# Kernel optimization log

Hardware: AMD Instinct MI355X
Metric: run time of the kernel (lower is better)

The kernel has to match this reference:

```python
import jax, jax.numpy as jnp
import numpy as np

B, T, D, H = 2048, 512, 1, 36


def _lstm_dir(x, Wih, Whh, bih, bhh, reverse):
    # x: [B,T,Din]; Wih: [4H,Din]; Whh: [4H,H]. PyTorch gate order: i,f,g,o.
    # Precompute input projection for all timesteps (hoisted out of the scan).
    xp = jnp.einsum('btd,gd->btg', x, Wih) + (bih + bhh)  # [B,T,4H]
    xp = jnp.swapaxes(xp, 0, 1)  # [T,B,4H]
    if reverse:
        xp = xp[::-1]
    h0 = jnp.zeros((x.shape[0], Whh.shape[1]), x.dtype)

    def step(carry, xt):
        h, c = carry
        z = xt + h @ Whh.T  # [B,4H]
        i, f, g, o = jnp.split(z, 4, axis=-1)
        c = jax.nn.sigmoid(f) * c + jax.nn.sigmoid(i) * jnp.tanh(g)
        h = jax.nn.sigmoid(o) * jnp.tanh(c)
        return (h, c), h

    _, hs = jax.lax.scan(step, (h0, h0), xp)  # hs: [T,B,H]
    if reverse:
        hs = hs[::-1]
    return jnp.swapaxes(hs, 0, 1)  # [B,T,H]


def _bilstm_layer(x, pf, pr):
    hf = _lstm_dir(x, *pf, reverse=False)
    hr = _lstm_dir(x, *pr, reverse=True)
    return jnp.concatenate([hf, hr], axis=-1)  # [B,T,2H]


def setup_inputs() -> dict:
    key = jax.random.key(0)
    ks = jax.random.split(key, 20)
    bound = 1.0 / np.sqrt(H)  # PyTorch LSTM/Linear uniform init bound

    def u(k, shape):
        return jax.random.uniform(k, shape, jnp.float32, -bound, bound)

    inp = {"x": jax.random.normal(ks[0], (B, T, D), jnp.float32)}
    # layer 0 (input size D), forward and reverse directions
    inp["Wih0f"] = u(ks[1], (4 * H, D)); inp["Whh0f"] = u(ks[2], (4 * H, H))
    inp["bih0f"] = u(ks[3], (4 * H,));  inp["bhh0f"] = u(ks[4], (4 * H,))
    inp["Wih0r"] = u(ks[5], (4 * H, D)); inp["Whh0r"] = u(ks[6], (4 * H, H))
    inp["bih0r"] = u(ks[7], (4 * H,));  inp["bhh0r"] = u(ks[8], (4 * H,))
    # layer 1 (input size 2H)
    inp["Wih1f"] = u(ks[9], (4 * H, 2 * H)); inp["Whh1f"] = u(ks[10], (4 * H, H))
    inp["bih1f"] = u(ks[11], (4 * H,));      inp["bhh1f"] = u(ks[12], (4 * H,))
    inp["Wih1r"] = u(ks[13], (4 * H, 2 * H)); inp["Whh1r"] = u(ks[14], (4 * H, H))
    inp["bih1r"] = u(ks[15], (4 * H,));       inp["bhh1r"] = u(ks[16], (4 * H,))
    # fc head: Linear(2H -> 1)
    inp["fcW"] = u(ks[17], (1, 2 * H))
    inp["fcb"] = u(ks[18], (1,))
    return inp


def reference(x, Wih0f, Whh0f, bih0f, bhh0f, Wih0r, Whh0r, bih0r, bhh0r,
              Wih1f, Whh1f, bih1f, bhh1f, Wih1r, Whh1r, bih1r, bhh1r,
              fcW, fcb):
    out = _bilstm_layer(x, (Wih0f, Whh0f, bih0f, bhh0f),
                        (Wih0r, Whh0r, bih0r, bhh0r))
    out = _bilstm_layer(out, (Wih1f, Whh1f, bih1f, bhh1f),
                        (Wih1r, Whh1r, bih1r, bhh1r))
    return out[:, -1, :] @ fcW.T + fcb  # [B,1]
```

## Files before the change

### kernel.cpp

```cpp
#include <hip/hip_runtime.h>
#include <cstdint>

#define Hn 36
#define G4 144
#define TT 512
#define BB 2048

__device__ __forceinline__ float sigf(float x) { return 1.0f / (1.0f + __expf(-x)); }
__device__ __forceinline__ float tanh_fast(float x) {
    float e = __expf(2.0f * x);
    return 1.0f - 2.0f / (e + 1.0f);
}

#define REP9(M, P)  M(P,0) M(P,1) M(P,2) M(P,3) M(P,4) M(P,5) M(P,6) M(P,7) M(P,8)
#define DECLQ(P, i) float P##i##x, P##i##y, P##i##z, P##i##w;
#define LOADQ(P, i) { float4 _t = wp[i]; P##i##x = _t.x; P##i##y = _t.y; P##i##z = _t.z; P##i##w = _t.w; }
#define PINQ(P, i)  asm volatile("" : "+v"(P##i##x), "+v"(P##i##y), "+v"(P##i##z), "+v"(P##i##w));
#define FMAQ(P, i)                                                        \
    {  float4 hv = *(const float4*)&hb[(i) * 4];                          \
       z0 = fmaf(P##i##x, hv.x, z0); z1 = fmaf(P##i##y, hv.y, z1);        \
       z2 = fmaf(P##i##z, hv.z, z2); z3 = fmaf(P##i##w, hv.w, z3); }

#define DOT4Q(P, i)                                                       \
    {   float4 hA = *(const float4*)&hbb[0 * 40 + (i) * 4];               \
        A0 = fmaf(P##i##x, hA.x, A0); A1 = fmaf(P##i##y, hA.y, A1);       \
        A2 = fmaf(P##i##z, hA.z, A2); A3 = fmaf(P##i##w, hA.w, A3);       \
        float4 hB = *(const float4*)&hbb[1 * 40 + (i) * 4];               \
        B0 = fmaf(P##i##x, hB.x, B0); B1 = fmaf(P##i##y, hB.y, B1);       \
        B2 = fmaf(P##i##z, hB.z, B2); B3 = fmaf(P##i##w, hB.w, B3);       \
        float4 hC = *(const float4*)&hbb[2 * 40 + (i) * 4];               \
        C0 = fmaf(P##i##x, hC.x, C0); C1 = fmaf(P##i##y, hC.y, C1);       \
        C2 = fmaf(P##i##z, hC.z, C2); C3 = fmaf(P##i##w, hC.w, C3);       \
        float4 hD = *(const float4*)&hbb[3 * 40 + (i) * 4];               \
        D0 = fmaf(P##i##x, hD.x, D0); D1 = fmaf(P##i##y, hD.y, D1);       \
        D2 = fmaf(P##i##z, hD.z, D2); D3 = fmaf(P##i##w, hD.w, D3); }

#define DOT36(W, H, Z0, Z1, Z2, Z3)                        \
    do {                                                   \
        _Pragma("unroll") for (int _k = 0; _k < 9; ++_k) { \
            float4 hv = *(const float4*)&(H)[_k * 4];      \
            Z0 = fmaf((W)[_k * 4 + 0], hv.x, Z0);          \
            Z1 = fmaf((W)[_k * 4 + 1], hv.y, Z1);          \
            Z2 = fmaf((W)[_k * 4 + 2], hv.z, Z2);          \
            Z3 = fmaf((W)[_k * 4 + 3], hv.w, Z3);          \
        }                                                  \
    } while (0)

#define DOT72(W, H, Z0, Z1, Z2, Z3)                         \
    do {                                                    \
        _Pragma("unroll") for (int _k = 0; _k < 18; ++_k) { \
            float4 hv = *(const float4*)&(H)[_k * 4];       \
            Z0 = fmaf((W)[_k * 4 + 0], hv.x, Z0);           \
            Z1 = fmaf((W)[_k * 4 + 1], hv.y, Z1);           \
            Z2 = fmaf((W)[_k * 4 + 2], hv.z, Z2);           \
            Z3 = fmaf((W)[_k * 4 + 3], hv.w, Z3);           \
        }                                                   \
    } while (0)

#define SG1 4
#define NTK1 (SG1 * G4)
__global__ __launch_bounds__(NTK1) void l0rev_kernel(
    const float* __restrict__ x,
    const float* __restrict__ Wih, const float* __restrict__ Whh,
    const float* __restrict__ bih, const float* __restrict__ bhh,
    float* __restrict__ h0r)
{
    const int tid = threadIdx.x;
    const int cc  = tid / G4;
    const int g   = tid % G4;
    const int b   = blockIdx.x * SG1 + cc;

    __shared__ float xs[SG1][TT];
    __shared__ float hs[SG1][40];
    __shared__ float zs[SG1][G4];

    for (int i = g; i < TT; i += G4) xs[cc][i] = x[(size_t)b * TT + i];

    REP9(DECLQ, R)
    {
        const float4* wp = (const float4*)(Whh + g * Hn);
        REP9(LOADQ, R)
    }
    float wx   = Wih[g];
    float bias = bih[g] + bhh[g];
    REP9(PINQ, R)
    asm volatile("" : "+v"(wx), "+v"(bias));

    if (g < 40) hs[cc][g] = 0.0f;
    float c = 0.0f;
    __syncthreads();

    float* dst = h0r + (size_t)b * TT * Hn;

    for (int s = 0; s < TT; ++s) {
        const int t = TT - 1 - s;
        float z0 = fmaf(xs[cc][t], wx, bias), z1 = 0.f, z2 = 0.f, z3 = 0.f;
        {
            const float* hb = hs[cc];
            REP9(FMAQ, R)
        }
        zs[cc][g] = (z0 + z1) + (z2 + z3);
        __syncthreads();
        if (g < Hn) {
            float zi = zs[cc][g], zf = zs[cc][g + 36], zg = zs[cc][g + 72], zo = zs[cc][g + 108];
            c = sigf(zf) * c + sigf(zi) * tanh_fast(zg);
            float h = sigf(zo) * tanh_fast(c);
            hs[cc][g] = h;
            dst[(size_t)t * Hn + g] = h;
        }
        __syncthreads();
    }
}

#define SG2 4
#define NT2 576
__global__ __launch_bounds__(NT2) void fused_fl_kernel(
    const float* __restrict__ x,
    const float* __restrict__ Wih0f, const float* __restrict__ Whh0f,
    const float* __restrict__ bih0f, const float* __restrict__ bhh0f,
    const float* __restrict__ Wih1f, const float* __restrict__ Whh1f,
    const float* __restrict__ bih1f, const float* __restrict__ bhh1f,
    const float* __restrict__ Wih1r,
    const float* __restrict__ bih1r, const float* __restrict__ bhh1r,
    const float* __restrict__ fcW, const float* __restrict__ fcb,
    const float* __restrict__ h0r,
    float* __restrict__ out)
{
    const int tid  = threadIdx.x;
    const int gp   = tid / G4;
    const int g    = tid % G4;
    const int cc2  = g / Hn;
    const int ii   = g % Hn;
    const int base = blockIdx.x * SG2;

    __shared__ float xs[SG2][TT + 2];
    __shared__ float h0f[2][SG2][40];
    __shared__ float h0rs[2][SG2][40];
    __shared__ float h1s[SG2][40];
    __shared__ float zF[SG2][G4];
    __shared__ float zL[3][SG2][G4];
    __shared__ float red[SG2][40];

    for (int i = tid; i < SG2 * (TT + 2); i += NT2) {
        int c = i / (TT + 2), t = i % (TT + 2);
        xs[c][t] = (t < TT) ? x[(size_t)(base + c) * TT + t] : 0.0f;
    }
    for (int i = tid; i < 2 * SG2 * 40; i += NT2) {
        (&h0f[0][0][0])[i] = 0.0f;
        (&h0rs[0][0][0])[i] = 0.0f;
    }
    for (int i = tid; i < SG2 * 40; i += NT2) (&h1s[0][0])[i] = 0.0f;

    const float* wbase = (gp == 0) ? (Whh0f + g * Hn)
                       : (gp == 1) ? (Wih1f + g * 72)
                       : (gp == 2) ? (Wih1f + g * 72 + 36)
                                   : (Whh1f + g * Hn);
    REP9(DECLQ, W)
    {
        const float4* wp = (const float4*)wbase;
        REP9(LOADQ, W)
    }
    float wx0  = (gp == 0) ? Wih0f[g] : 0.0f;
    float bsum = (gp == 0) ? (bih0f[g] + bhh0f[g])
               : (gp == 3) ? (bih1f[g] + bhh1f[g]) : 0.0f;
    REP9(PINQ, W)
    asm volatile("" : "+v"(wx0), "+v"(bsum));

    const float* srow = h0r + (size_t)(base + cc2) * TT * Hn + ii;
    float c0 = 0.0f, c1 = 0.0f;
    __syncthreads();

    float rv = 0.0f;
    if (gp == 0) {
#pragma unroll
        for (int c = 0; c < SG2; ++c) zF[c][g] = fmaf(xs[c][0], wx0, bsum);
    } else if (gp == 2) {
        h0rs[0][cc2][ii] = srow[0];
        rv = srow[Hn];
    }
    __syncthreads();
    if (gp == 0) {
        float zi = zF[cc2][ii], zg = zF[cc2][ii + 72], zo = zF[cc2][ii + 108];
        c0 = sigf(zi) * tanh_fast(zg);
        h0f[0][cc2][ii] = sigf(zo) * tanh_fast(c0);
    }
    __syncthreads();

    int cur = 0;
    for (int t = 0; t < TT; ++t) {
        float rv2 = (gp == 2 && t + 2 < TT) ? srow[(size_t)(t + 2) * Hn] : 0.0f;

        const float* hbb = (gp <= 1) ? &h0f[cur][0][0]
                         : (gp == 2) ? &h0rs[cur][0][0] : &h1s[0][0];
        float A0, B0, C0, D0;
        if (gp == 0) {
            A0 = fmaf(xs[0][t + 1], wx0, bsum);
            B0 = fmaf(xs[1][t + 1], wx0, bsum);
            C0 = fmaf(xs[2][t + 1], wx0, bsum);
            D0 = fmaf(xs[3][t + 1], wx0, bsum);
        } else {
            A0 = bsum; B0 = bsum; C0 = bsum; D0 = bsum;
        }
        float A1 = 0.f, A2 = 0.f, A3 = 0.f, B1 = 0.f, B2 = 0.f, B3 = 0.f;
        float C1 = 0.f, C2 = 0.f, C3 = 0.f, D1 = 0.f, D2 = 0.f, D3 = 0.f;

        REP9(DOT4Q, W)

        float zA = (A0 + A1) + (A2 + A3);
        float zB = (B0 + B1) + (B2 + B3);
        float zC = (C0 + C1) + (C2 + C3);
        float zD = (D0 + D1) + (D2 + D3);
        if (gp == 0) {
            zF[0][g] = zA; zF[1][g] = zB; zF[2][g] = zC; zF[3][g] = zD;
        } else {
            float* zt = &zL[gp - 1][0][0];
            zt[0 * G4 + g] = zA; zt[1 * G4 + g] = zB;
            zt[2 * G4 + g] = zC; zt[3 * G4 + g] = zD;
        }
        __syncthreads();

        if (gp == 0) {
            if (t + 1 < TT) {
                float zi = zF[cc2][ii],       zf = zF[cc2][ii + 36];
                float zg = zF[cc2][ii + 72],  zo = zF[cc2][ii + 108];
                c0 = sigf(zf) * c0 + sigf(zi) * tanh_fast(zg);
                h0f[cur ^ 1][cc2][ii] = sigf(zo) * tanh_fast(c0);
            }
        } else if (gp == 3) {
            float zi = zL[0][cc2][ii]       + zL[1][cc2][ii]       + zL[2][cc2][ii];
            float zf = zL[0][cc2][ii + 36]  + zL[1][cc2][ii + 36]  + zL[2][cc2][ii + 36];
            float zg = zL[0][cc2][ii + 72]  + zL[1][cc2][ii + 72]  + zL[2][cc2][ii + 72];
            float zo = zL[0][cc2][ii + 108] + zL[1][cc2][ii + 108] + zL[2][cc2][ii + 108];
            c1 = sigf(zf) * c1 + sigf(zi) * tanh_fast(zg);
            h1s[cc2][ii] = sigf(zo) * tanh_fast(c1);
        } else if (gp == 2 && t + 1 < TT) {
            h0rs[cur ^ 1][cc2][ii] = rv;
        }
        __syncthreads();
        rv = rv2;
        if (t + 1 < TT) cur ^= 1;
    }

    {
        float zR = bih1r[g] + bhh1r[g];
        const float* wr = Wih1r + g * 72;
#pragma unroll
        for (int k = 0; k < Hn; ++k) zR = fmaf(wr[k],      h0f[cur][gp][k],  zR);
#pragma unroll
        for (int k = 0; k < Hn; ++k) zR = fmaf(wr[36 + k], h0rs[cur][gp][k], zR);
        zF[gp][g] = zR;
    }
    __syncthreads();
    if (tid < SG2 * Hn) {
        int c = tid / Hn, i = tid % Hn;
        float zi = zF[c][i], zg = zF[c][i + 72], zo = zF[c][i + 108];
        float cR = sigf(zi) * tanh_fast(zg);
        float hR = sigf(zo) * tanh_fast(cR);
        red[c][i] = fcW[36 + i] * hR + fcW[i] * h1s[c][i];
    }
    __syncthreads();
    if (tid < SG2) {
        float s2 = fcb[0];
        for (int j = 0; j < Hn; ++j) s2 += red[tid][j];
        out[base + tid] = s2;
    }
}

__global__ __launch_bounds__(G4, 1) void fused_all_kernel(
    const float* __restrict__ x,
    const float* __restrict__ Wih0f, const float* __restrict__ Whh0f,
    const float* __restrict__ bih0f, const float* __restrict__ bhh0f,
    const float* __restrict__ Wih0r, const float* __restrict__ Whh0r,
    const float* __restrict__ bih0r, const float* __restrict__ bhh0r,
    const float* __restrict__ Wih1f, const float* __restrict__ Whh1f,
    const float* __restrict__ bih1f, const float* __restrict__ bhh1f,
    const float* __restrict__ Wih1r,
    const float* __restrict__ bih1r, const float* __restrict__ bhh1r,
    const float* __restrict__ fcW, const float* __restrict__ fcb,
    float* __restrict__ out)
{
    const int g = threadIdx.x;
    const int b = blockIdx.x;

    __shared__ float xs[TT];
    __shared__ float cbuf[64][Hn];
    __shared__ float ckpt_h[8][Hn], ckpt_c[8][Hn];
    __shared__ float hr[40], h0s[80], hs1[40], zs[G4], red[40];

    for (int i = g; i < TT; i += G4) xs[i] = x[(size_t)b * TT + i];

    float wr[Hn], wf[Hn];
#pragma unroll
    for (int k = 0; k < Hn; ++k) wr[k] = Whh0r[g * Hn + k];
#pragma unroll
    for (int k = 0; k < Hn; ++k) wf[k] = Whh0f[g * Hn + k];
    const float wxr = Wih0r[g], br = bih0r[g] + bhh0r[g];
    const float wxf = Wih0f[g], bf = bih0f[g] + bhh0f[g];
    float w1i[72];
#pragma unroll
    for (int k = 0; k < 72; ++k) w1i[k] = Wih1f[g * 72 + k];
    float w1h[Hn];
#pragma unroll
    for (int k = 0; k < Hn; ++k) w1h[k] = Whh1f[g * Hn + k];
    const float b1 = bih1f[g] + bhh1f[g];

    if (g < Hn) hr[g] = 0.0f;
    float cr = 0.0f;
    __syncthreads();
    for (int s = 0; s < TT; ++s) {
        const int t = TT - 1 - s;
        if ((t & 63) == 63 && g < Hn) { ckpt_h[t >> 6][g] = hr[g]; ckpt_c[t >> 6][g] = cr; }
        float z0 = fmaf(xs[t], wxr, br), z1 = 0.f, z2 = 0.f, z3 = 0.f;
        DOT36(wr, hr, z0, z1, z2, z3);
        zs[g] = (z0 + z1) + (z2 + z3);
        __syncthreads();
        if (g < Hn) {
            float zi = zs[g], zf = zs[g + 36], zg = zs[g + 72], zo = zs[g + 108];
            cr = sigf(zf) * cr + sigf(zi) * tanh_fast(zg);
            hr[g] = sigf(zo) * tanh_fast(cr);
        }
        __syncthreads();
    }

    if (g < Hn) { h0s[g] = 0.0f; hs1[g] = 0.0f; }
    float c0 = 0.0f, c1 = 0.0f;
    __syncthreads();

    for (int m = 0; m < 8; ++m) {
        if (g < Hn) { hr[g] = ckpt_h[m][g]; cr = ckpt_c[m][g]; }
        __syncthreads();
        for (int j = 0; j < 64; ++j) {
            const int t = m * 64 + 63 - j;
            float z0 = fmaf(xs[t], wxr, br), z1 = 0.f, z2 = 0.f, z3 = 0.f;
            DOT36(wr, hr, z0, z1, z2, z3);
            zs[g] = (z0 + z1) + (z2 + z3);
            __syncthreads();
            if (g < Hn) {
                float zi = zs[g], zf = zs[g + 36], zg = zs[g + 72], zo = zs[g + 108];
                cr = sigf(zf) * cr + sigf(zi) * tanh_fast(zg);
                float h = sigf(zo) * tanh_fast(cr);
                hr[g] = h;
                cbuf[t & 63][g] = h;
            }
            __syncthreads();
        }
        for (int j = 0; j < 64; ++j) {
            const int t = m * 64 + j;
            float z0 = fmaf(xs[t], wxf, bf), z1 = 0.f, z2 = 0.f, z3 = 0.f;
            DOT36(wf, h0s, z0, z1, z2, z3);
            zs[g] = (z0 + z1) + (z2 + z3);
            __syncthreads();
            if (g < Hn) {
                float zi = zs[g], zf = zs[g + 36], zg = zs[g + 72], zo = zs[g + 108];
                c0 = sigf(zf) * c0 + sigf(zi) * tanh_fast(zg);
                h0s[g] = sigf(zo) * tanh_fast(c0);
            } else if (g < 72) {
                h0s[g] = cbuf[j][g - 36];
            }
            __syncthreads();
            float y0 = b1, y1 = 0.f, y2 = 0.f, y3 = 0.f;
            DOT72(w1i, h0s, y0, y1, y2, y3);
            DOT36(w1h, hs1, y0, y1, y2, y3);
            zs[g] = (y0 + y1) + (y2 + y3);
            __syncthreads();
            if (g < Hn) {
                float zi = zs[g], zf = zs[g + 36], zg = zs[g + 72], zo = zs[g + 108];
                c1 = sigf(zf) * c1 + sigf(zi) * tanh_fast(zg);
                hs1[g] = sigf(zo) * tanh_fast(c1);
            }
            __syncthreads();
        }
    }

    float zR = bih1r[g] + bhh1r[g];
#pragma unroll
    for (int k = 0; k < 72; ++k) zR = fmaf(Wih1r[g * 72 + k], h0s[k], zR);
    zs[g] = zR;
    __syncthreads();
    if (g < Hn) {
        float zi = zs[g], zg = zs[g + 72], zo = zs[g + 108];
        float c  = sigf(zi) * tanh_fast(zg);
        float hrv = sigf(zo) * tanh_fast(c);
        red[g] = fcW[36 + g] * hrv + fcW[g] * hs1[g];
    }
    __syncthreads();
    if (g == 0) {
        float s = fcb[0];
        for (int j = 0; j < Hn; ++j) s += red[j];
        out[b] = s;
    }
}

extern "C" void kernel_launch(void* const* d_in, const int* in_sizes, int n_in,
                              void* d_out, int out_size, void* d_ws, size_t ws_size,
                              hipStream_t stream)
{
    const float* x     = (const float*)d_in[0];
    const float* Wih0f = (const float*)d_in[1];
    const float* Whh0f = (const float*)d_in[2];
    const float* bih0f = (const float*)d_in[3];
    const float* bhh0f = (const float*)d_in[4];
    const float* Wih0r = (const float*)d_in[5];
    const float* Whh0r = (const float*)d_in[6];
    const float* bih0r = (const float*)d_in[7];
    const float* bhh0r = (const float*)d_in[8];
    const float* Wih1f = (const float*)d_in[9];
    const float* Whh1f = (const float*)d_in[10];
    const float* bih1f = (const float*)d_in[11];
    const float* bhh1f = (const float*)d_in[12];
    const float* Wih1r = (const float*)d_in[13];
    const float* bih1r = (const float*)d_in[15];
    const float* bhh1r = (const float*)d_in[16];
    const float* fcW   = (const float*)d_in[17];
    const float* fcb   = (const float*)d_in[18];

    const size_t need = (size_t)BB * TT * Hn * sizeof(float);
    if (d_ws != nullptr && ws_size >= need) {
        float* h0r = (float*)d_ws;
        l0rev_kernel<<<BB / SG1, NTK1, 0, stream>>>(x, Wih0r, Whh0r, bih0r, bhh0r, h0r);
        fused_fl_kernel<<<BB / SG2, NT2, 0, stream>>>(
            x, Wih0f, Whh0f, bih0f, bhh0f, Wih1f, Whh1f, bih1f, bhh1f,
            Wih1r, bih1r, bhh1r, fcW, fcb, h0r, (float*)d_out);
    } else {
        fused_all_kernel<<<BB, G4, 0, stream>>>(
            x, Wih0f, Whh0f, bih0f, bhh0f, Wih0r, Whh0r, bih0r, bhh0r,
            Wih1f, Whh1f, bih1f, bhh1f, Wih1r, bih1r, bhh1r, fcW, fcb,
            (float*)d_out);
    }
}
```

Baseline: 2.036 ms.

## Process eight sequences per block with weights staged in shared memory

Doubles the sequences handled per block of the fused forward/layer-1 kernel from four to eight, so each weight load feeds eight dot products. Weight rows move from pinned registers into shared memory (with a padded stride for the Wih1 rows). The gate-activation work is reassigned so that the first 288 threads handle layer-0 forward cells and the rest handle layer-1 cells plus staging of the reverse hidden state, with the tail computation split into two sub-sequences per group. This halves the grid to 256 blocks. It adds LDS traffic for the weights and raises register and LDS pressure, which may lower occupancy.

```diff
diff --git a/kernel.cpp b/kernel.cpp
--- a/kernel.cpp
+++ b/kernel.cpp
@@ -20,20 +20,6 @@
     {  float4 hv = *(const float4*)&hb[(i) * 4];                          \
        z0 = fmaf(P##i##x, hv.x, z0); z1 = fmaf(P##i##y, hv.y, z1);        \
        z2 = fmaf(P##i##z, hv.z, z2); z3 = fmaf(P##i##w, hv.w, z3); }
-
-#define DOT4Q(P, i)                                                       \
-    {   float4 hA = *(const float4*)&hbb[0 * 40 + (i) * 4];               \
-        A0 = fmaf(P##i##x, hA.x, A0); A1 = fmaf(P##i##y, hA.y, A1);       \
-        A2 = fmaf(P##i##z, hA.z, A2); A3 = fmaf(P##i##w, hA.w, A3);       \
-        float4 hB = *(const float4*)&hbb[1 * 40 + (i) * 4];               \
-        B0 = fmaf(P##i##x, hB.x, B0); B1 = fmaf(P##i##y, hB.y, B1);       \
-        B2 = fmaf(P##i##z, hB.z, B2); B3 = fmaf(P##i##w, hB.w, B3);       \
-        float4 hC = *(const float4*)&hbb[2 * 40 + (i) * 4];               \
-        C0 = fmaf(P##i##x, hC.x, C0); C1 = fmaf(P##i##y, hC.y, C1);       \
-        C2 = fmaf(P##i##z, hC.z, C2); C3 = fmaf(P##i##w, hC.w, C3);       \
-        float4 hD = *(const float4*)&hbb[3 * 40 + (i) * 4];               \
-        D0 = fmaf(P##i##x, hD.x, D0); D1 = fmaf(P##i##y, hD.y, D1);       \
-        D2 = fmaf(P##i##z, hD.z, D2); D3 = fmaf(P##i##w, hD.w, D3); }
 
 #define DOT36(W, H, Z0, Z1, Z2, Z3)                        \
     do {                                                   \
@@ -112,8 +98,39 @@
     }
 }
 
-#define SG2 4
-#define NT2 576
+#define SG2  8
+#define NT2  576
+#define NB2  (BB / SG2)
+#define W1ST 76
+
+#define DOT8Q(i)                                                              \
+    {   float4 wq = *(const float4*)&wrow[(i) * 4];                           \
+        float4 hq;                                                            \
+        hq = *(const float4*)&hbb[0 * 40 + (i) * 4];                          \
+        A0 = fmaf(wq.x, hq.x, A0); A1 = fmaf(wq.y, hq.y, A1);                 \
+        A2 = fmaf(wq.z, hq.z, A2); A3 = fmaf(wq.w, hq.w, A3);                 \
+        hq = *(const float4*)&hbb[1 * 40 + (i) * 4];                          \
+        B0 = fmaf(wq.x, hq.x, B0); B1 = fmaf(wq.y, hq.y, B1);                 \
+        B2 = fmaf(wq.z, hq.z, B2); B3 = fmaf(wq.w, hq.w, B3);                 \
+        hq = *(const float4*)&hbb[2 * 40 + (i) * 4];                          \
+        C0 = fmaf(wq.x, hq.x, C0); C1 = fmaf(wq.y, hq.y, C1);                 \
+        C2 = fmaf(wq.z, hq.z, C2); C3 = fmaf(wq.w, hq.w, C3);                 \
+        hq = *(const float4*)&hbb[3 * 40 + (i) * 4];                          \
+        D0 = fmaf(wq.x, hq.x, D0); D1 = fmaf(wq.y, hq.y, D1);                 \
+        D2 = fmaf(wq.z, hq.z, D2); D3 = fmaf(wq.w, hq.w, D3);                 \
+        hq = *(const float4*)&hbb[4 * 40 + (i) * 4];                          \
+        E0 = fmaf(wq.x, hq.x, E0); E1 = fmaf(wq.y, hq.y, E1);                 \
+        E2 = fmaf(wq.z, hq.z, E2); E3 = fmaf(wq.w, hq.w, E3);                 \
+        hq = *(const float4*)&hbb[5 * 40 + (i) * 4];                          \
+        F0 = fmaf(wq.x, hq.x, F0); F1 = fmaf(wq.y, hq.y, F1);                 \
+        F2 = fmaf(wq.z, hq.z, F2); F3 = fmaf(wq.w, hq.w, F3);                 \
+        hq = *(const float4*)&hbb[6 * 40 + (i) * 4];                          \
+        G0 = fmaf(wq.x, hq.x, G0); G1 = fmaf(wq.y, hq.y, G1);                 \
+        G2 = fmaf(wq.z, hq.z, G2); G3 = fmaf(wq.w, hq.w, G3);                 \
+        hq = *(const float4*)&hbb[7 * 40 + (i) * 4];                          \
+        H0 = fmaf(wq.x, hq.x, H0); H1 = fmaf(wq.y, hq.y, H1);                 \
+        H2 = fmaf(wq.z, hq.z, H2); H3 = fmaf(wq.w, hq.w, H3); }
+
 __global__ __launch_bounds__(NT2) void fused_fl_kernel(
     const float* __restrict__ x,
     const float* __restrict__ Wih0f, const float* __restrict__ Whh0f,
@@ -129,18 +146,28 @@
     const int tid  = threadIdx.x;
     const int gp   = tid / G4;
     const int g    = tid % G4;
-    const int cc2  = g / Hn;
-    const int ii   = g % Hn;
     const int base = blockIdx.x * SG2;
-
+    const int ca = tid / Hn;
+    const int ia = tid % Hn;
+    const int ct = tid - 288;
+    const int cb = (ct >= 0) ? ct / Hn : 0;
+    const int ib = (ct >= 0) ? ct % Hn : 0;
+
+    __shared__ float wt0[G4 * 36];
+    __shared__ float wt1[G4 * W1ST];
+    __shared__ float wt3[G4 * 36];
     __shared__ float xs[SG2][TT + 2];
     __shared__ float h0f[2][SG2][40];
     __shared__ float h0rs[2][SG2][40];
     __shared__ float h1s[SG2][40];
     __shared__ float zF[SG2][G4];
     __shared__ float zL[3][SG2][G4];
-    __shared__ float red[SG2][40];
-
+    __shared__ float red[SG2][Hn];
+
+    for (int i = tid; i < G4 * 36; i += NT2) wt0[i] = Whh0f[i];
+    for (int i = tid; i < G4 * 72; i += NT2)
+        wt1[(i / 72) * W1ST + (i % 72)] = Wih1f[i];
+    for (int i = tid; i < G4 * 36; i += NT2) wt3[i] = Whh1f[i];
     for (int i = tid; i < SG2 * (TT + 2); i += NT2) {
         int c = i / (TT + 2), t = i % (TT + 2);
         xs[c][t] = (t < TT) ? x[(size_t)(base + c) * TT + t] : 0.0f;
@@ -151,112 +178,112 @@
     }
     for (int i = tid; i < SG2 * 40; i += NT2) (&h1s[0][0])[i] = 0.0f;
 
-    const float* wbase = (gp == 0) ? (Whh0f + g * Hn)
-                       : (gp == 1) ? (Wih1f + g * 72)
-                       : (gp == 2) ? (Wih1f + g * 72 + 36)
-                                   : (Whh1f + g * Hn);
-    REP9(DECLQ, W)
-    {
-        const float4* wp = (const float4*)wbase;
-        REP9(LOADQ, W)
-    }
-    float wx0  = (gp == 0) ? Wih0f[g] : 0.0f;
-    float bsum = (gp == 0) ? (bih0f[g] + bhh0f[g])
-               : (gp == 3) ? (bih1f[g] + bhh1f[g]) : 0.0f;
-    REP9(PINQ, W)
-    asm volatile("" : "+v"(wx0), "+v"(bsum));
-
-    const float* srow = h0r + (size_t)(base + cc2) * TT * Hn + ii;
-    float c0 = 0.0f, c1 = 0.0f;
-    __syncthreads();
-
-    float rv = 0.0f;
+    const float* wrow = (gp == 0) ? &wt0[g * 36]
+                      : (gp == 1) ? &wt1[g * W1ST]
+                      : (gp == 2) ? &wt1[g * W1ST + 36]
+                                  : &wt3[g * 36];
+    const float wx0  = (gp == 0) ? Wih0f[g] : 0.0f;
+    const float bsum = (gp == 0) ? (bih0f[g] + bhh0f[g])
+                     : (gp == 3) ? (bih1f[g] + bhh1f[g]) : 0.0f;
+
+    const float* srow = h0r + (size_t)(base + cb) * TT * Hn + ib;
+    float c0 = 0.0f, c1 = 0.0f, rvv = 0.0f;
+    __syncthreads();
+
     if (gp == 0) {
 #pragma unroll
         for (int c = 0; c < SG2; ++c) zF[c][g] = fmaf(xs[c][0], wx0, bsum);
-    } else if (gp == 2) {
-        h0rs[0][cc2][ii] = srow[0];
-        rv = srow[Hn];
-    }
-    __syncthreads();
-    if (gp == 0) {
-        float zi = zF[cc2][ii], zg = zF[cc2][ii + 72], zo = zF[cc2][ii + 108];
+    }
+    if (ct >= 0) {
+        h0rs[0][cb][ib] = srow[0];
+        rvv = srow[Hn];
+    }
+    __syncthreads();
+    if (tid < 288) {
+        float zi = zF[ca][ia], zg = zF[ca][ia + 72], zo = zF[ca][ia + 108];
         c0 = sigf(zi) * tanh_fast(zg);
-        h0f[0][cc2][ii] = sigf(zo) * tanh_fast(c0);
+        h0f[0][ca][ia] = sigf(zo) * tanh_fast(c0);
     }
     __syncthreads();
 
     int cur = 0;
     for (int t = 0; t < TT; ++t) {
-        float rv2 = (gp == 2 && t + 2 < TT) ? srow[(size_t)(t + 2) * Hn] : 0.0f;
+        float rv2 = (ct >= 0 && t + 2 < TT) ? srow[(size_t)(t + 2) * Hn] : 0.0f;
 
         const float* hbb = (gp <= 1) ? &h0f[cur][0][0]
                          : (gp == 2) ? &h0rs[cur][0][0] : &h1s[0][0];
-        float A0, B0, C0, D0;
+        float A0, B0, C0, D0, E0, F0, G0, H0;
         if (gp == 0) {
             A0 = fmaf(xs[0][t + 1], wx0, bsum);
             B0 = fmaf(xs[1][t + 1], wx0, bsum);
             C0 = fmaf(xs[2][t + 1], wx0, bsum);
             D0 = fmaf(xs[3][t + 1], wx0, bsum);
+            E0 = fmaf(xs[4][t + 1], wx0, bsum);
+            F0 = fmaf(xs[5][t + 1], wx0, bsum);
+            G0 = fmaf(xs[6][t + 1], wx0, bsum);
+            H0 = fmaf(xs[7][t + 1], wx0, bsum);
         } else {
             A0 = bsum; B0 = bsum; C0 = bsum; D0 = bsum;
+            E0 = bsum; F0 = bsum; G0 = bsum; H0 = bsum;
         }
         float A1 = 0.f, A2 = 0.f, A3 = 0.f, B1 = 0.f, B2 = 0.f, B3 = 0.f;
         float C1 = 0.f, C2 = 0.f, C3 = 0.f, D1 = 0.f, D2 = 0.f, D3 = 0.f;
-
-        REP9(DOT4Q, W)
-
-        float zA = (A0 + A1) + (A2 + A3);
-        float zB = (B0 + B1) + (B2 + B3);
-        float zC = (C0 + C1) + (C2 + C3);
-        float zD = (D0 + D1) + (D2 + D3);
-        if (gp == 0) {
-            zF[0][g] = zA; zF[1][g] = zB; zF[2][g] = zC; zF[3][g] = zD;
+        float E1 = 0.f, E2 = 0.f, E3 = 0.f, F1 = 0.f, F2 = 0.f, F3 = 0.f;
+        float G1 = 0.f, G2 = 0.f, G3 = 0.f, H1 = 0.f, H2 = 0.f, H3 = 0.f;
+
+        DOT8Q(0) DOT8Q(1) DOT8Q(2) DOT8Q(3) DOT8Q(4)
+        DOT8Q(5) DOT8Q(6) DOT8Q(7) DOT8Q(8)
+
+        float zA = (A0 + A1) + (A2 + A3), zB = (B0 + B1) + (B2 + B3);
+        float zC = (C0 + C1) + (C2 + C3), zD = (D0 + D1) + (D2 + D3);
+        float zE = (E0 + E1) + (E2 + E3), zF_ = (F0 + F1) + (F2 + F3);
+        float zG = (G0 + G1) + (G2 + G3), zH = (H0 + H1) + (H2 + H3);
+        float* zt = (gp == 0) ? &zF[0][0] : &zL[gp - 1][0][0];
+        zt[0 * G4 + g] = zA; zt[1 * G4 + g] = zB; zt[2 * G4 + g] = zC;
+        zt[3 * G4 + g] = zD; zt[4 * G4 + g] = zE; zt[5 * G4 + g] = zF_;
+        zt[6 * G4 + g] = zG; zt[7 * G4 + g] = zH;
+        __syncthreads();
+
+        if (tid < 288) {
+            if (t + 1 < TT) {
+                float zi = zF[ca][ia],       zf = zF[ca][ia + 36];
+                float zg = zF[ca][ia + 72],  zo = zF[ca][ia + 108];
+                c0 = sigf(zf) * c0 + sigf(zi) * tanh_fast(zg);
+                h0f[cur ^ 1][ca][ia] = sigf(zo) * tanh_fast(c0);
+            }
         } else {
-            float* zt = &zL[gp - 1][0][0];
-            zt[0 * G4 + g] = zA; zt[1 * G4 + g] = zB;
-            zt[2 * G4 + g] = zC; zt[3 * G4 + g] = zD;
-        }
-        __syncthreads();
-
-        if (gp == 0) {
-            if (t + 1 < TT) {
-                float zi = zF[cc2][ii],       zf = zF[cc2][ii + 36];
-                float zg = zF[cc2][ii + 72],  zo = zF[cc2][ii + 108];
-                c0 = sigf(zf) * c0 + sigf(zi) * tanh_fast(zg);
-                h0f[cur ^ 1][cc2][ii] = sigf(zo) * tanh_fast(c0);
-            }
-        } else if (gp == 3) {
-            float zi = zL[0][cc2][ii]       + zL[1][cc2][ii]       + zL[2][cc2][ii];
-            float zf = zL[0][cc2][ii + 36]  + zL[1][cc2][ii + 36]  + zL[2][cc2][ii + 36];
-            float zg = zL[0][cc2][ii + 72]  + zL[1][cc2][ii + 72]  + zL[2][cc2][ii + 72];
-            float zo = zL[0][cc2][ii + 108] + zL[1][cc2][ii + 108] + zL[2][cc2][ii + 108];
+            float zi = zL[0][cb][ib]       + zL[1][cb][ib]       + zL[2][cb][ib];
+            float zf = zL[0][cb][ib + 36]  + zL[1][cb][ib + 36]  + zL[2][cb][ib + 36];
+            float zg = zL[0][cb][ib + 72]  + zL[1][cb][ib + 72]  + zL[2][cb][ib + 72];
+            float zo = zL[0][cb][ib + 108] + zL[1][cb][ib + 108] + zL[2][cb][ib + 108];
             c1 = sigf(zf) * c1 + sigf(zi) * tanh_fast(zg);
-            h1s[cc2][ii] = sigf(zo) * tanh_fast(c1);
-        } else if (gp == 2 && t + 1 < TT) {
-            h0rs[cur ^ 1][cc2][ii] = rv;
-        }
-        __syncthreads();
-        rv = rv2;
+            h1s[cb][ib] = sigf(zo) * tanh_fast(c1);
+            if (t + 1 < TT) h0rs[cur ^ 1][cb][ib] = rvv;
+        }
+        __syncthreads();
+        rvv = rv2;
         if (t + 1 < TT) cur ^= 1;
     }
 
     {
-        float zR = bih1r[g] + bhh1r[g];
-        const float* wr = Wih1r + g * 72;
-#pragma unroll
-        for (int k = 0; k < Hn; ++k) zR = fmaf(wr[k],      h0f[cur][gp][k],  zR);
-#pragma unroll
-        for (int k = 0; k < Hn; ++k) zR = fmaf(wr[36 + k], h0rs[cur][gp][k], zR);
-        zF[gp][g] = zR;
-    }
-    __syncthreads();
-    if (tid < SG2 * Hn) {
-        int c = tid / Hn, i = tid % Hn;
-        float zi = zF[c][i], zg = zF[c][i + 72], zo = zF[c][i + 108];
+#pragma unroll
+        for (int sub = 0; sub < 2; ++sub) {
+            const int cc = gp * 2 + sub;
+            float zR = bih1r[g] + bhh1r[g];
+            const float* wr = Wih1r + g * 72;
+#pragma unroll
+            for (int k = 0; k < Hn; ++k) zR = fmaf(wr[k],      h0f[cur][cc][k],  zR);
+#pragma unroll
+            for (int k = 0; k < Hn; ++k) zR = fmaf(wr[36 + k], h0rs[cur][cc][k], zR);
+            zF[cc][g] = zR;
+        }
+    }
+    __syncthreads();
+    if (tid < 288) {
+        float zi = zF[ca][ia], zg = zF[ca][ia + 72], zo = zF[ca][ia + 108];
         float cR = sigf(zi) * tanh_fast(zg);
         float hR = sigf(zo) * tanh_fast(cR);
-        red[c][i] = fcW[36 + i] * hR + fcW[i] * h1s[c][i];
+        red[ca][ia] = fcW[36 + ia] * hR + fcW[ia] * h1s[ca][ia];
     }
     __syncthreads();
     if (tid < SG2) {
@@ -418,7 +445,7 @@
     if (d_ws != nullptr && ws_size >= need) {
         float* h0r = (float*)d_ws;
         l0rev_kernel<<<BB / SG1, NTK1, 0, stream>>>(x, Wih0r, Whh0r, bih0r, bhh0r, h0r);
-        fused_fl_kernel<<<BB / SG2, NT2, 0, stream>>>(
+        fused_fl_kernel<<<NB2, NT2, 0, stream>>>(
             x, Wih0f, Whh0f, bih0f, bhh0f, Wih1f, Whh1f, bih1f, bhh1f,
             Wih1r, bih1r, bhh1r, fcW, fcb, h0r, (float*)d_out);
     } else {
```

Measured after the change: 2.005 ms. About the same (-1.5%).

## Ping-pong two sequence groups per block with weights staged in LDS

Applied to the files above, without the earlier changes.

The fused forward/layer-1 kernel now handles 8 sequences per block, split into two halves of 4. Each timestep interleaves them: while one half's gate dot products run, the other half's nonlinear combine runs, which drops the double-buffered h state. Recurrent and input weights move from pinned registers into transposed float4 tiles in shared memory to make room for the second half, and the grid is halved. This hides the serial combine phase behind the dot-product work, at the cost of more LDS traffic per FMA, higher LDS use that may limit occupancy, and fewer blocks.

```diff
diff --git a/kernel.cpp b/kernel.cpp
--- a/kernel.cpp
+++ b/kernel.cpp
@@ -20,20 +20,6 @@
     {  float4 hv = *(const float4*)&hb[(i) * 4];                          \
        z0 = fmaf(P##i##x, hv.x, z0); z1 = fmaf(P##i##y, hv.y, z1);        \
        z2 = fmaf(P##i##z, hv.z, z2); z3 = fmaf(P##i##w, hv.w, z3); }
-
-#define DOT4Q(P, i)                                                       \
-    {   float4 hA = *(const float4*)&hbb[0 * 40 + (i) * 4];               \
-        A0 = fmaf(P##i##x, hA.x, A0); A1 = fmaf(P##i##y, hA.y, A1);       \
-        A2 = fmaf(P##i##z, hA.z, A2); A3 = fmaf(P##i##w, hA.w, A3);       \
-        float4 hB = *(const float4*)&hbb[1 * 40 + (i) * 4];               \
-        B0 = fmaf(P##i##x, hB.x, B0); B1 = fmaf(P##i##y, hB.y, B1);       \
-        B2 = fmaf(P##i##z, hB.z, B2); B3 = fmaf(P##i##w, hB.w, B3);       \
-        float4 hC = *(const float4*)&hbb[2 * 40 + (i) * 4];               \
-        C0 = fmaf(P##i##x, hC.x, C0); C1 = fmaf(P##i##y, hC.y, C1);       \
-        C2 = fmaf(P##i##z, hC.z, C2); C3 = fmaf(P##i##w, hC.w, C3);       \
-        float4 hD = *(const float4*)&hbb[3 * 40 + (i) * 4];               \
-        D0 = fmaf(P##i##x, hD.x, D0); D1 = fmaf(P##i##y, hD.y, D1);       \
-        D2 = fmaf(P##i##z, hD.z, D2); D3 = fmaf(P##i##w, hD.w, D3); }
 
 #define DOT36(W, H, Z0, Z1, Z2, Z3)                        \
     do {                                                   \
@@ -112,8 +98,10 @@
     }
 }
 
-#define SG2 4
-#define NT2 576
+#define SG2  8
+#define NT2  576
+#define NB2  (BB / SG2)
+
 __global__ __launch_bounds__(NT2) void fused_fl_kernel(
     const float* __restrict__ x,
     const float* __restrict__ Wih0f, const float* __restrict__ Whh0f,
@@ -129,134 +117,182 @@
     const int tid  = threadIdx.x;
     const int gp   = tid / G4;
     const int g    = tid % G4;
-    const int cc2  = g / Hn;
-    const int ii   = g % Hn;
     const int base = blockIdx.x * SG2;
-
+    const int cA = (tid < 144) ? tid / 36 : 0;
+    const int uA = (tid < 144) ? tid % 36 : 0;
+    const int cB = (tid >= 144 && tid < 288) ? (tid - 144) / 36 : 0;
+    const int uB = (tid >= 144 && tid < 288) ? (tid - 144) % 36 : 0;
+    const int cs = (tid >= 288 && tid < 432) ? (tid - 288) / 36 : 0;
+    const int us = (tid >= 288 && tid < 432) ? (tid - 288) % 36 : 0;
+
+    __shared__ float4 wt0t[9 * G4];
+    __shared__ float4 wt1t[18 * G4];
+    __shared__ float4 wt3t[9 * G4];
     __shared__ float xs[SG2][TT + 2];
-    __shared__ float h0f[2][SG2][40];
-    __shared__ float h0rs[2][SG2][40];
+    __shared__ float h0f[SG2][40];
+    __shared__ float h0rs[SG2][40];
     __shared__ float h1s[SG2][40];
     __shared__ float zF[SG2][G4];
     __shared__ float zL[3][SG2][G4];
-    __shared__ float red[SG2][40];
-
+    __shared__ float red[SG2][Hn];
+
+    for (int i = tid; i < 9 * G4; i += NT2) {
+        int q = i / G4, r = i % G4;
+        wt0t[q * G4 + r] = ((const float4*)(Whh0f + r * Hn))[q];
+        wt3t[q * G4 + r] = ((const float4*)(Whh1f + r * Hn))[q];
+    }
+    for (int i = tid; i < 18 * G4; i += NT2) {
+        int q = i / G4, r = i % G4;
+        wt1t[q * G4 + r] = ((const float4*)(Wih1f + r * 72))[q];
+    }
     for (int i = tid; i < SG2 * (TT + 2); i += NT2) {
         int c = i / (TT + 2), t = i % (TT + 2);
         xs[c][t] = (t < TT) ? x[(size_t)(base + c) * TT + t] : 0.0f;
     }
-    for (int i = tid; i < 2 * SG2 * 40; i += NT2) {
-        (&h0f[0][0][0])[i] = 0.0f;
-        (&h0rs[0][0][0])[i] = 0.0f;
-    }
-    for (int i = tid; i < SG2 * 40; i += NT2) (&h1s[0][0])[i] = 0.0f;
-
-    const float* wbase = (gp == 0) ? (Whh0f + g * Hn)
-                       : (gp == 1) ? (Wih1f + g * 72)
-                       : (gp == 2) ? (Wih1f + g * 72 + 36)
-                                   : (Whh1f + g * Hn);
-    REP9(DECLQ, W)
+    for (int i = tid; i < SG2 * 40; i += NT2) {
+        (&h0f[0][0])[i] = 0.0f;
+        (&h0rs[0][0])[i] = 0.0f;
+        (&h1s[0][0])[i] = 0.0f;
+    }
+
+    const float4* wb4 = (gp == 0) ? wt0t
+                      : (gp == 1) ? wt1t
+                      : (gp == 2) ? (wt1t + 9 * G4)
+                                  : wt3t;
+    const float wx0  = (gp == 0) ? Wih0f[g] : 0.0f;
+    const float bsum = (gp == 0) ? (bih0f[g] + bhh0f[g])
+                     : (gp == 3) ? (bih1f[g] + bhh1f[g]) : 0.0f;
+
+    const float* srowA = h0r + (size_t)(base + cs) * TT * Hn + us;
+    const float* srowB = h0r + (size_t)(base + 4 + cs) * TT * Hn + us;
+    float c0A = 0.f, c0B = 0.f, c1A = 0.f, c1B = 0.f, rvA = 0.f, rvB = 0.f;
+    __syncthreads();
+
+    if (gp == 0) {
+#pragma unroll
+        for (int ci = 0; ci < SG2; ++ci)
+            zF[ci][g] = fmaf(xs[ci][0], wx0, bsum);
+    }
+    if (tid >= 288 && tid < 432) {
+        h0rs[cs][us]     = srowA[0];
+        h0rs[4 + cs][us] = srowB[0];
+        rvA = srowA[Hn];
+        rvB = srowB[Hn];
+    }
+    __syncthreads();
+    if (tid < 144) {
+        {   float zi = zF[cA][uA], zg = zF[cA][uA + 72], zo = zF[cA][uA + 108];
+            c0A = sigf(zi) * tanh_fast(zg);
+            h0f[cA][uA] = sigf(zo) * tanh_fast(c0A); }
+        {   float zi = zF[4 + cA][uA], zg = zF[4 + cA][uA + 72], zo = zF[4 + cA][uA + 108];
+            c0B = sigf(zi) * tanh_fast(zg);
+            h0f[4 + cA][uA] = sigf(zo) * tanh_fast(c0B); }
+    }
+    __syncthreads();
+
+#define DOT_PHASE(CH0)                                                        \
+    {   const float* hbb = (gp <= 1) ? &h0f[CH0][0]                           \
+                         : (gp == 2) ? &h0rs[CH0][0] : &h1s[CH0][0];          \
+        float A0, B0, C0, D0;                                                 \
+        if (gp == 0) {                                                        \
+            A0 = fmaf(xs[CH0 + 0][t + 1], wx0, bsum);                         \
+            B0 = fmaf(xs[CH0 + 1][t + 1], wx0, bsum);                         \
+            C0 = fmaf(xs[CH0 + 2][t + 1], wx0, bsum);                         \
+            D0 = fmaf(xs[CH0 + 3][t + 1], wx0, bsum);                         \
+        } else { A0 = bsum; B0 = bsum; C0 = bsum; D0 = bsum; }                \
+        float A1 = 0.f, A2 = 0.f, A3 = 0.f, B1 = 0.f, B2 = 0.f, B3 = 0.f;     \
+        float C1 = 0.f, C2 = 0.f, C3 = 0.f, D1 = 0.f, D2 = 0.f, D3 = 0.f;     \
+        _Pragma("unroll")                                                     \
+        for (int i = 0; i < 9; ++i) {                                         \
+            float4 w = wb4[i * G4 + g];                                       \
+            float4 h;                                                         \
+            h = *(const float4*)&hbb[0 * 40 + i * 4];                         \
+            A0 = fmaf(w.x, h.x, A0); A1 = fmaf(w.y, h.y, A1);                 \
+            A2 = fmaf(w.z, h.z, A2); A3 = fmaf(w.w, h.w, A3);                 \
+            h = *(const float4*)&hbb[1 * 40 + i * 4];                         \
+            B0 = fmaf(w.x, h.x, B0); B1 = fmaf(w.y, h.y, B1);                 \
+            B2 = fmaf(w.z, h.z, B2); B3 = fmaf(w.w, h.w, B3);                 \
+            h = *(const float4*)&hbb[2 * 40 + i * 4];                         \
+            C0 = fmaf(w.x, h.x, C0); C1 = fmaf(w.y, h.y, C1);                 \
+            C2 = fmaf(w.z, h.z, C2); C3 = fmaf(w.w, h.w, C3);                 \
+            h = *(const float4*)&hbb[3 * 40 + i * 4];                         \
+            D0 = fmaf(w.x, h.x, D0); D1 = fmaf(w.y, h.y, D1);                 \
+            D2 = fmaf(w.z, h.z, D2); D3 = fmaf(w.w, h.w, D3);                 \
+        }                                                                     \
+        float* zt = (gp == 0) ? &zF[CH0][0] : &zL[gp - 1][CH0][0];            \
+        zt[0 * G4 + g] = (A0 + A1) + (A2 + A3);                               \
+        zt[1 * G4 + g] = (B0 + B1) + (B2 + B3);                               \
+        zt[2 * G4 + g] = (C0 + C1) + (C2 + C3);                               \
+        zt[3 * G4 + g] = (D0 + D1) + (D2 + D3);                               \
+    }
+
+#define L0_COMBINE(CH0, CREG, WRITE_H)                                        \
+    {   float zi = zF[(CH0) + cA][uA],       zf = zF[(CH0) + cA][uA + 36];    \
+        float zg = zF[(CH0) + cA][uA + 72],  zo = zF[(CH0) + cA][uA + 108];   \
+        CREG = sigf(zf) * CREG + sigf(zi) * tanh_fast(zg);                    \
+        if (WRITE_H) h0f[(CH0) + cA][uA] = sigf(zo) * tanh_fast(CREG);        \
+    }
+
+#define L1_COMBINE(CH0, CREG)                                                 \
+    {   float zi = zL[0][(CH0) + cB][uB]       + zL[1][(CH0) + cB][uB]       + zL[2][(CH0) + cB][uB];       \
+        float zf = zL[0][(CH0) + cB][uB + 36]  + zL[1][(CH0) + cB][uB + 36]  + zL[2][(CH0) + cB][uB + 36];  \
+        float zg = zL[0][(CH0) + cB][uB + 72]  + zL[1][(CH0) + cB][uB + 72]  + zL[2][(CH0) + cB][uB + 72];  \
+        float zo = zL[0][(CH0) + cB][uB + 108] + zL[1][(CH0) + cB][uB + 108] + zL[2][(CH0) + cB][uB + 108]; \
+        CREG = sigf(zf) * CREG + sigf(zi) * tanh_fast(zg);                    \
+        h1s[(CH0) + cB][uB] = sigf(zo) * tanh_fast(CREG);                     \
+    }
+
+    for (int t = 0; t < TT; ++t) {
+        if (t > 0) {
+            if (tid < 144) {
+                L0_COMBINE(4, c0B, true)
+            } else if (tid < 288) {
+                L1_COMBINE(4, c1B)
+            } else if (tid < 432) {
+                h0rs[4 + cs][us] = rvB;
+                rvB = (t + 1 < TT) ? srowB[(size_t)(t + 1) * Hn] : 0.0f;
+            }
+        }
+        DOT_PHASE(0)
+        __syncthreads();
+
+        if (tid < 144) {
+            L0_COMBINE(0, c0A, (t + 1 < TT))
+        } else if (tid < 288) {
+            L1_COMBINE(0, c1A)
+        } else if (tid < 432) {
+            if (t + 1 < TT) h0rs[cs][us] = rvA;
+            rvA = (t + 2 < TT) ? srowA[(size_t)(t + 2) * Hn] : 0.0f;
+        }
+        DOT_PHASE(4)
+        __syncthreads();
+    }
+    if (tid >= 144 && tid < 288) {
+        L1_COMBINE(4, c1B)
+    }
+    __syncthreads();
+
     {
-        const float4* wp = (const float4*)wbase;
-        REP9(LOADQ, W)
-    }
-    float wx0  = (gp == 0) ? Wih0f[g] : 0.0f;
-    float bsum = (gp == 0) ? (bih0f[g] + bhh0f[g])
-               : (gp == 3) ? (bih1f[g] + bhh1f[g]) : 0.0f;
-    REP9(PINQ, W)
-    asm volatile("" : "+v"(wx0), "+v"(bsum));
-
-    const float* srow = h0r + (size_t)(base + cc2) * TT * Hn + ii;
-    float c0 = 0.0f, c1 = 0.0f;
-    __syncthreads();
-
-    float rv = 0.0f;
-    if (gp == 0) {
-#pragma unroll
-        for (int c = 0; c < SG2; ++c) zF[c][g] = fmaf(xs[c][0], wx0, bsum);
-    } else if (gp == 2) {
-        h0rs[0][cc2][ii] = srow[0];
-        rv = srow[Hn];
-    }
-    __syncthreads();
-    if (gp == 0) {
-        float zi = zF[cc2][ii], zg = zF[cc2][ii + 72], zo = zF[cc2][ii + 108];
-        c0 = sigf(zi) * tanh_fast(zg);
-        h0f[0][cc2][ii] = sigf(zo) * tanh_fast(c0);
-    }
-    __syncthreads();
-
-    int cur = 0;
-    for (int t = 0; t < TT; ++t) {
-        float rv2 = (gp == 2 && t + 2 < TT) ? srow[(size_t)(t + 2) * Hn] : 0.0f;
-
-        const float* hbb = (gp <= 1) ? &h0f[cur][0][0]
-                         : (gp == 2) ? &h0rs[cur][0][0] : &h1s[0][0];
-        float A0, B0, C0, D0;
-        if (gp == 0) {
-            A0 = fmaf(xs[0][t + 1], wx0, bsum);
-            B0 = fmaf(xs[1][t + 1], wx0, bsum);
-            C0 = fmaf(xs[2][t + 1], wx0, bsum);
-            D0 = fmaf(xs[3][t + 1], wx0, bsum);
-        } else {
-            A0 = bsum; B0 = bsum; C0 = bsum; D0 = bsum;
-        }
-        float A1 = 0.f, A2 = 0.f, A3 = 0.f, B1 = 0.f, B2 = 0.f, B3 = 0.f;
-        float C1 = 0.f, C2 = 0.f, C3 = 0.f, D1 = 0.f, D2 = 0.f, D3 = 0.f;
-
-        REP9(DOT4Q, W)
-
-        float zA = (A0 + A1) + (A2 + A3);
-        float zB = (B0 + B1) + (B2 + B3);
-        float zC = (C0 + C1) + (C2 + C3);
-        float zD = (D0 + D1) + (D2 + D3);
-        if (gp == 0) {
-            zF[0][g] = zA; zF[1][g] = zB; zF[2][g] = zC; zF[3][g] = zD;
-        } else {
-            float* zt = &zL[gp - 1][0][0];
-            zt[0 * G4 + g] = zA; zt[1 * G4 + g] = zB;
-            zt[2 * G4 + g] = zC; zt[3 * G4 + g] = zD;
-        }
-        __syncthreads();
-
-        if (gp == 0) {
-            if (t + 1 < TT) {
-                float zi = zF[cc2][ii],       zf = zF[cc2][ii + 36];
-                float zg = zF[cc2][ii + 72],  zo = zF[cc2][ii + 108];
-                c0 = sigf(zf) * c0 + sigf(zi) * tanh_fast(zg);
-                h0f[cur ^ 1][cc2][ii] = sigf(zo) * tanh_fast(c0);
-            }
-        } else if (gp == 3) {
-            float zi = zL[0][cc2][ii]       + zL[1][cc2][ii]       + zL[2][cc2][ii];
-            float zf = zL[0][cc2][ii + 36]  + zL[1][cc2][ii + 36]  + zL[2][cc2][ii + 36];
-            float zg = zL[0][cc2][ii + 72]  + zL[1][cc2][ii + 72]  + zL[2][cc2][ii + 72];
-            float zo = zL[0][cc2][ii + 108] + zL[1][cc2][ii + 108] + zL[2][cc2][ii + 108];
-            c1 = sigf(zf) * c1 + sigf(zi) * tanh_fast(zg);
-            h1s[cc2][ii] = sigf(zo) * tanh_fast(c1);
-        } else if (gp == 2 && t + 1 < TT) {
-            h0rs[cur ^ 1][cc2][ii] = rv;
-        }
-        __syncthreads();
-        rv = rv2;
-        if (t + 1 < TT) cur ^= 1;
-    }
-
-    {
-        float zR = bih1r[g] + bhh1r[g];
-        const float* wr = Wih1r + g * 72;
-#pragma unroll
-        for (int k = 0; k < Hn; ++k) zR = fmaf(wr[k],      h0f[cur][gp][k],  zR);
-#pragma unroll
-        for (int k = 0; k < Hn; ++k) zR = fmaf(wr[36 + k], h0rs[cur][gp][k], zR);
-        zF[gp][g] = zR;
-    }
-    __syncthreads();
-    if (tid < SG2 * Hn) {
-        int c = tid / Hn, i = tid % Hn;
-        float zi = zF[c][i], zg = zF[c][i + 72], zo = zF[c][i + 108];
+        const int gpT = tid / G4, gT = tid % G4;
+#pragma unroll
+        for (int s2 = 0; s2 < 2; ++s2) {
+            const int cc = gpT * 2 + s2;
+            float zR = bih1r[gT] + bhh1r[gT];
+            const float* wrq = Wih1r + gT * 72;
+#pragma unroll
+            for (int k = 0; k < Hn; ++k) zR = fmaf(wrq[k],      h0f[cc][k],  zR);
+#pragma unroll
+            for (int k = 0; k < Hn; ++k) zR = fmaf(wrq[36 + k], h0rs[cc][k], zR);
+            zF[cc][gT] = zR;
+        }
+    }
+    __syncthreads();
+    if (tid < 288) {
+        const int c2 = tid / 36, i2 = tid % 36;
+        float zi = zF[c2][i2], zg = zF[c2][i2 + 72], zo = zF[c2][i2 + 108];
         float cR = sigf(zi) * tanh_fast(zg);
         float hR = sigf(zo) * tanh_fast(cR);
-        red[c][i] = fcW[36 + i] * hR + fcW[i] * h1s[c][i];
+        red[c2][i2] = fcW[36 + i2] * hR + fcW[i2] * h1s[c2][i2];
     }
     __syncthreads();
     if (tid < SG2) {
@@ -264,6 +300,9 @@
         for (int j = 0; j < Hn; ++j) s2 += red[tid][j];
         out[base + tid] = s2;
     }
+#undef DOT_PHASE
+#undef L0_COMBINE
+#undef L1_COMBINE
 }
 
 __global__ __launch_bounds__(G4, 1) void fused_all_kernel(
@@ -418,7 +457,7 @@
     if (d_ws != nullptr && ws_size >= need) {
         float* h0r = (float*)d_ws;
         l0rev_kernel<<<BB / SG1, NTK1, 0, stream>>>(x, Wih0r, Whh0r, bih0r, bhh0r, h0r);
-        fused_fl_kernel<<<BB / SG2, NT2, 0, stream>>>(
+        fused_fl_kernel<<<NB2, NT2, 0, stream>>>(
             x, Wih0f, Whh0f, bih0f, bhh0f, Wih1f, Whh1f, bih1f, bhh1f,
             Wih1r, bih1r, bhh1r, fcW, fcb, h0r, (float*)d_out);
     } else {
```

Measured after the change: 1.901 ms. 6.7% less time.
